# Performance work log

Hardware: AMD Instinct MI355X
Metric: run time of the kernel (lower is better)

The kernel has to match this reference:

```python
import jax, jax.numpy as jnp
import numpy as np

CH = 512      # input channels
V = 320       # codewords per group
G = 2         # groups
CV_DIM = 256  # codevector_dim (wav2vec2 default)
D = CV_DIM // G
TAU = 2.0     # gumbel temperature


def setup_inputs() -> dict:
    key = jax.random.key(0)
    k1, k2, k3, k4 = jax.random.split(key, 4)
    B, T = 32, 1024
    x = jax.random.normal(k1, (B, T, CH), jnp.float32)
    W_proj = jax.random.normal(k2, (CH, G * V), jnp.float32) / np.sqrt(CH)
    b_proj = jnp.zeros((G * V,), jnp.float32)
    codevectors = jax.random.normal(k3, (G, V, D), jnp.float32) * 0.02
    # uniform noise, transformed to Gumbel inside reference
    u_noise = jax.random.uniform(k4, (B, T, G, V), jnp.float32,
                                 minval=1e-6, maxval=1.0 - 1e-6)
    return {"x": x, "W_proj": W_proj, "b_proj": b_proj,
            "codevectors": codevectors, "u_noise": u_noise}


def reference(x, W_proj, b_proj, codevectors, u_noise):
    B, T, _ = x.shape
    # projection to per-group logits: [B,T,G,V]
    logits = (x @ W_proj + b_proj).reshape(B, T, G, V)
    # gumbel-softmax (hard, straight-through)
    g = -jnp.log(-jnp.log(u_noise))
    soft = jax.nn.softmax((logits + g) / TAU, axis=-1)
    hard = jax.nn.one_hot(jnp.argmax(soft, axis=-1), V, dtype=soft.dtype)
    st = hard + soft - jax.lax.stop_gradient(soft)
    # combine selected codewords per group, concat groups -> [B,T,CV_DIM]
    out = jnp.einsum('btgv,gvd->btgd', st, codevectors).reshape(B, T, G * D)
    return out
```

## Files before the change

kernel.cpp:

```cpp
#include <hip/hip_runtime.h>
#include <cmath>

namespace {

typedef _Float16 half8 __attribute__((ext_vector_type(8)));
typedef float f32x4 __attribute__((ext_vector_type(4)));

constexpr int M_TOTAL = 32 * 1024;
constexpr int K_CH    = 512;
constexpr int NV      = 640;
constexpr int D_CV    = 128;
constexpr int NSLOT   = 10;

constexpr int BM = 128, BN = 128, BK = 32;
constexpr int NTILE  = NV / BN;
constexpr int NPANEL = M_TOTAL / BM;
constexpr int NBLK   = NTILE * NPANEL;
constexpr int KT     = K_CH / BK;

constexpr float LO_SCALE = 4096.0f;
constexpr float LO_INV   = 1.0f / 4096.0f;

__device__ __forceinline__ void gld16(const void* g, void* l) {
  __builtin_amdgcn_global_load_lds(
      (__attribute__((address_space(1))) void*)g,
      (__attribute__((address_space(3))) void*)l, 16, 0, 0);
}

__global__ __launch_bounds__(256)
void prep_w(const float* __restrict__ W, _Float16* __restrict__ Wth,
            _Float16* __restrict__ Wtl)
{
  __shared__ float tile[32][33];
  const int bk = blockIdx.x & 15;
  const int bn = blockIdx.x >> 4;
  const int k0 = bk * 32, n0 = bn * 32;
  const int t = threadIdx.x;
  const int nn = t & 31, kk = t >> 5;
  #pragma unroll
  for (int p = 0; p < 4; ++p)
    tile[kk + p * 8][nn] = W[(size_t)(k0 + kk + p * 8) * NV + n0 + nn];
  __syncthreads();
  const int kx = t & 31, nx = t >> 5;
  #pragma unroll
  for (int p = 0; p < 4; ++p) {
    const float v = tile[kx][nx + p * 8];
    const _Float16 h = (_Float16)v;
    const _Float16 l = (_Float16)((v - (float)h) * LO_SCALE);
    const size_t o = (size_t)(n0 + nx + p * 8) * K_CH + k0 + kx;
    Wth[o] = h;
    Wtl[o] = l;
  }
}

__global__ __launch_bounds__(256, 2)
void gvq_mfma12(const float* __restrict__ x,
                const _Float16* __restrict__ Wth, const _Float16* __restrict__ Wtl,
                const float* __restrict__ bias, const float* __restrict__ u,
                float* __restrict__ pval, int* __restrict__ pidx)
{
  __shared__ __align__(16) char lds[2][32768];

  const int chunk = NBLK / 8;
  const int nid   = (blockIdx.x % 8) * chunk + blockIdx.x / 8;
  const int panel = nid / NTILE, ntile = nid % NTILE;
  const int m0 = panel * BM, n0 = ntile * BN;

  const int t    = threadIdx.x;
  const int wv   = t >> 6, lane = t & 63;
  const int wr   = wv >> 1, wc = wv & 1;
  const int li   = lane & 15, q = lane >> 4;

  const int gca = (t & 7) ^ ((t >> 3) & 7);
  const float* pxa = x + (size_t)(m0 + (t >> 3)) * K_CH + gca * 4;
  const int gcb = (t & 3) ^ ((t >> 3) & 3);
  const _Float16* pbh = Wth + (size_t)(n0 + (t >> 2)) * K_CH + gcb * 8;
  const _Float16* pbl = Wtl + (size_t)(n0 + (t >> 2)) * K_CH + gcb * 8;

  f32x4 acc1[4][4];
  f32x4 acc2[4][4];
  #pragma unroll
  for (int i = 0; i < 4; ++i)
    #pragma unroll
    for (int j = 0; j < 4; ++j) {
      acc1[i][j] = (f32x4){0.f, 0.f, 0.f, 0.f};
      acc2[i][j] = (f32x4){0.f, 0.f, 0.f, 0.f};
    }

  auto stage = [&](int kt, int b) {
    const int ko = kt * BK;
    char* L = lds[b];
    #pragma unroll
    for (int i = 0; i < 4; ++i)
      gld16(pxa + (size_t)i * 32 * K_CH + ko, L + i * 4096 + wv * 1024);
    #pragma unroll
    for (int i = 0; i < 2; ++i) {
      gld16(pbh + (size_t)i * 64 * K_CH + ko, L + 16384 + i * 4096 + wv * 1024);
      gld16(pbl + (size_t)i * 64 * K_CH + ko, L + 24576 + i * 4096 + wv * 1024);
    }
  };

  const int abase = (wr * 64 + li) * 128;
  const int s0 = (((q * 2 + 0) ^ (li & 7)) << 4);
  const int s1 = (((q * 2 + 1) ^ (li & 7)) << 4);
  const int bboff = (wc * 64 + li) * 64 + ((q ^ ((li >> 1) & 3)) << 4);

  stage(0, 0);
  stage(1, 1);
  #pragma unroll
  for (int kt = 0; kt < KT; ++kt) {
    const int cur = kt & 1;
    if (kt < KT - 1) asm volatile("s_waitcnt vmcnt(8)" ::: "memory");
    else             asm volatile("s_waitcnt vmcnt(0)" ::: "memory");
    __builtin_amdgcn_s_barrier();
    __builtin_amdgcn_sched_barrier(0);

    const char* L = lds[cur];
    half8 bh[4], bl[4];
    f32x4 af0[4], af1[4];
    #pragma unroll
    for (int fn = 0; fn < 4; ++fn) {
      bh[fn] = *reinterpret_cast<const half8*>(L + 16384 + fn * 1024 + bboff);
      bl[fn] = *reinterpret_cast<const half8*>(L + 24576 + fn * 1024 + bboff);
    }
    #pragma unroll
    for (int fm = 0; fm < 4; ++fm) {
      af0[fm] = *reinterpret_cast<const f32x4*>(L + abase + fm * 2048 + s0);
      af1[fm] = *reinterpret_cast<const f32x4*>(L + abase + fm * 2048 + s1);
    }
    #pragma unroll
    for (int fm = 0; fm < 4; ++fm) {
      half8 ah, al;
      #pragma unroll
      for (int e = 0; e < 4; ++e) {
        const float v0 = af0[fm][e], v1 = af1[fm][e];
        const _Float16 h0 = (_Float16)v0, h1 = (_Float16)v1;
        ah[e]     = h0; al[e]     = (_Float16)((v0 - (float)h0) * LO_SCALE);
        ah[4 + e] = h1; al[4 + e] = (_Float16)((v1 - (float)h1) * LO_SCALE);
      }
      #pragma unroll
      for (int fn = 0; fn < 4; ++fn) {
        acc1[fm][fn] = __builtin_amdgcn_mfma_f32_16x16x32_f16(
            ah, bh[fn], acc1[fm][fn], 0, 0, 0);
        acc2[fm][fn] = __builtin_amdgcn_mfma_f32_16x16x32_f16(
            ah, bl[fn], acc2[fm][fn], 0, 0, 0);
        acc2[fm][fn] = __builtin_amdgcn_mfma_f32_16x16x32_f16(
            al, bh[fn], acc2[fm][fn], 0, 0, 0);
      }
    }
    __builtin_amdgcn_s_barrier();
    __builtin_amdgcn_sched_barrier(0);
    if (kt + 2 < KT) stage(kt + 2, cur);
  }

  const int colbase = n0 + wc * 64 + li;
  float bb[4];
  #pragma unroll
  for (int fn = 0; fn < 4; ++fn) bb[fn] = bias[colbase + fn * 16];

  const int slot = ntile * 2 + wc;
  #pragma unroll
  for (int fm = 0; fm < 4; ++fm) {
    #pragma unroll
    for (int r = 0; r < 4; ++r) {
      const int m = m0 + wr * 64 + fm * 16 + q * 4 + r;
      float bv = -INFINITY;
      int   bi = 0x7fffffff;
      #pragma unroll
      for (int fn = 0; fn < 4; ++fn) {
        const float uu  = u[(size_t)m * NV + colbase + fn * 16];
        const float g   = -__logf(-__logf(uu));
        const float val = acc1[fm][fn][r] + acc2[fm][fn][r] * LO_INV
                          + bb[fn] + g;
        const int   n   = colbase + fn * 16;
        if (val > bv) { bv = val; bi = n; }
      }
      #pragma unroll
      for (int s = 1; s <= 8; s <<= 1) {
        const float ov = __shfl_xor(bv, s);
        const int   oi = __shfl_xor(bi, s);
        if (ov > bv || (ov == bv && oi < bi)) { bv = ov; bi = oi; }
      }
      if (li == 0) {
        pval[(size_t)m * NSLOT + slot] = bv;
        pidx[(size_t)m * NSLOT + slot] = bi;
      }
    }
  }
}

__global__ __launch_bounds__(256)
void gvq_gather(const float* __restrict__ pval,
                const int*   __restrict__ pidx,
                const float* __restrict__ cv,
                float* __restrict__ out)
{
  const int tid  = threadIdx.x;
  const int w    = tid >> 6;
  const int lane = tid & 63;
  const int m    = blockIdx.x * 4 + w;
  const int g    = lane >> 5;

  const float* pv = &pval[(size_t)m * NSLOT + g * 5];
  const int*   pi = &pidx[(size_t)m * NSLOT + g * 5];
  float bv = pv[0];
  int   bi = pi[0];
  #pragma unroll
  for (int s = 1; s < 5; ++s) {
    const float v = pv[s];
    const int   i = pi[s];
    if (v > bv || (v == bv && i < bi)) { bv = v; bi = i; }
  }
  const float4 src = *reinterpret_cast<const float4*>(
      &cv[(size_t)bi * D_CV + (lane & 31) * 4]);
  *reinterpret_cast<float4*>(&out[(size_t)m * 256 + lane * 4]) = src;
}

}

extern "C" void kernel_launch(void* const* d_in, const int* in_sizes, int n_in,
                              void* d_out, int out_size, void* d_ws, size_t ws_size,
                              hipStream_t stream)
{
  const float* x    = (const float*)d_in[0];
  const float* W    = (const float*)d_in[1];
  const float* bias = (const float*)d_in[2];
  const float* cv   = (const float*)d_in[3];
  const float* u    = (const float*)d_in[4];
  float* out = (float*)d_out;

  _Float16* Wth  = (_Float16*)d_ws;
  _Float16* Wtl  = Wth + (size_t)NV * K_CH;
  float*    pval = (float*)(Wtl + (size_t)NV * K_CH);
  int*      pidx = (int*)(pval + (size_t)M_TOTAL * NSLOT);

  hipLaunchKernelGGL(prep_w, dim3(320), dim3(256), 0, stream, W, Wth, Wtl);
  hipLaunchKernelGGL(gvq_mfma12, dim3(NBLK), dim3(256), 0, stream,
                     x, Wth, Wtl, bias, u, pval, pidx);
  hipLaunchKernelGGL(gvq_gather, dim3(M_TOTAL / 4), dim3(256), 0, stream,
                     pval, pidx, cv, out);
}
```

Measured before the change: 123.7 us.

## Replace split-fp16 GEMM with single fp16 pass plus fp32 fixup of near-ties

Drops the hi/lo fp16 split that needed three MFMAs per tile and computes logits with one fp16 MFMA, converting x to fp16 in registers before writing it to LDS. It also doubles BK. To keep the argmax correct, the kernel tracks the runner-up value per row. Rows whose top-two margin is within a tolerance are appended to a list via an atomic counter, and a fix kernel recomputes their logits in fp32. This cuts MFMA work roughly threefold and halves B traffic. The cost is two extra launches, a memset, and correctness that depends on the tolerance bounding the fp16 error.

```diff
diff --git a/kernel.cpp b/kernel.cpp
--- a/kernel.cpp
+++ b/kernel.cpp
@@ -12,14 +12,13 @@
 constexpr int D_CV    = 128;
 constexpr int NSLOT   = 10;
 
-constexpr int BM = 128, BN = 128, BK = 32;
+constexpr int BM = 128, BN = 128, BK = 64;
 constexpr int NTILE  = NV / BN;
 constexpr int NPANEL = M_TOTAL / BM;
 constexpr int NBLK   = NTILE * NPANEL;
 constexpr int KT     = K_CH / BK;
 
-constexpr float LO_SCALE = 4096.0f;
-constexpr float LO_INV   = 1.0f / 4096.0f;
+constexpr float TAU = 6e-3f;
 
 __device__ __forceinline__ void gld16(const void* g, void* l) {
   __builtin_amdgcn_global_load_lds(
@@ -28,8 +27,8 @@
 }
 
 __global__ __launch_bounds__(256)
-void prep_w(const float* __restrict__ W, _Float16* __restrict__ Wth,
-            _Float16* __restrict__ Wtl)
+void prep_w2(const float* __restrict__ W, _Float16* __restrict__ Wth,
+             float* __restrict__ Wtf)
 {
   __shared__ float tile[32][33];
   const int bk = blockIdx.x & 15;
@@ -45,19 +44,17 @@
   #pragma unroll
   for (int p = 0; p < 4; ++p) {
     const float v = tile[kx][nx + p * 8];
-    const _Float16 h = (_Float16)v;
-    const _Float16 l = (_Float16)((v - (float)h) * LO_SCALE);
     const size_t o = (size_t)(n0 + nx + p * 8) * K_CH + k0 + kx;
-    Wth[o] = h;
-    Wtl[o] = l;
+    Wth[o] = (_Float16)v;
+    Wtf[o] = v;
   }
 }
 
 __global__ __launch_bounds__(256, 2)
-void gvq_mfma12(const float* __restrict__ x,
-                const _Float16* __restrict__ Wth, const _Float16* __restrict__ Wtl,
-                const float* __restrict__ bias, const float* __restrict__ u,
-                float* __restrict__ pval, int* __restrict__ pidx)
+void gvq_p1(const float* __restrict__ x, const _Float16* __restrict__ Wth,
+            const float* __restrict__ bias, const float* __restrict__ u,
+            float* __restrict__ pval, int* __restrict__ pidx,
+            float* __restrict__ psec)
 {
   __shared__ __align__(16) char lds[2][32768];
 
@@ -71,86 +68,81 @@
   const int wr   = wv >> 1, wc = wv & 1;
   const int li   = lane & 15, q = lane >> 4;
 
-  const int gca = (t & 7) ^ ((t >> 3) & 7);
-  const float* pxa = x + (size_t)(m0 + (t >> 3)) * K_CH + gca * 4;
-  const int gcb = (t & 3) ^ ((t >> 3) & 3);
-  const _Float16* pbh = Wth + (size_t)(n0 + (t >> 2)) * K_CH + gcb * 8;
-  const _Float16* pbl = Wtl + (size_t)(n0 + (t >> 2)) * K_CH + gcb * 8;
-
-  f32x4 acc1[4][4];
-  f32x4 acc2[4][4];
+  const int ar0   = t >> 3;
+  const int aslot = (t & 7) ^ ((t >> 3) & 7);
+  const float* pxa = x + (size_t)(m0 + ar0) * K_CH + (t & 7) * 8;
+  const int bgc = (t & 7) ^ ((t >> 3) & 7);
+  const _Float16* pbh = Wth + (size_t)(n0 + (t >> 3)) * K_CH + bgc * 8;
+
+  f32x4 acc[4][4];
   #pragma unroll
   for (int i = 0; i < 4; ++i)
     #pragma unroll
-    for (int j = 0; j < 4; ++j) {
-      acc1[i][j] = (f32x4){0.f, 0.f, 0.f, 0.f};
-      acc2[i][j] = (f32x4){0.f, 0.f, 0.f, 0.f};
-    }
-
-  auto stage = [&](int kt, int b) {
-    const int ko = kt * BK;
-    char* L = lds[b];
+    for (int j = 0; j < 4; ++j) acc[i][j] = (f32x4){0.f, 0.f, 0.f, 0.f};
+
+  f32x4 aR[8];
+  auto issueA = [&](int kt) {
     #pragma unroll
     for (int i = 0; i < 4; ++i)
-      gld16(pxa + (size_t)i * 32 * K_CH + ko, L + i * 4096 + wv * 1024);
-    #pragma unroll
-    for (int i = 0; i < 2; ++i) {
-      gld16(pbh + (size_t)i * 64 * K_CH + ko, L + 16384 + i * 4096 + wv * 1024);
-      gld16(pbl + (size_t)i * 64 * K_CH + ko, L + 24576 + i * 4096 + wv * 1024);
-    }
+      #pragma unroll
+      for (int j = 0; j < 2; ++j)
+        aR[i * 2 + j] = *reinterpret_cast<const f32x4*>(
+            pxa + (size_t)i * 32 * K_CH + kt * BK + j * 4);
   };
-
-  const int abase = (wr * 64 + li) * 128;
-  const int s0 = (((q * 2 + 0) ^ (li & 7)) << 4);
-  const int s1 = (((q * 2 + 1) ^ (li & 7)) << 4);
-  const int bboff = (wc * 64 + li) * 64 + ((q ^ ((li >> 1) & 3)) << 4);
-
-  stage(0, 0);
-  stage(1, 1);
+  auto issueB = [&](int kt, int b) {
+    char* Lb = lds[b] + 16384;
+    #pragma unroll
+    for (int i = 0; i < 4; ++i)
+      gld16(pbh + (size_t)i * 32 * K_CH + kt * BK, Lb + i * 4096 + wv * 1024);
+  };
+  auto writeA = [&](int b) {
+    char* La = lds[b];
+    #pragma unroll
+    for (int i = 0; i < 4; ++i) {
+      half8 h;
+      #pragma unroll
+      for (int e = 0; e < 4; ++e) {
+        h[e]     = (_Float16)aR[i * 2][e];
+        h[4 + e] = (_Float16)aR[i * 2 + 1][e];
+      }
+      *reinterpret_cast<half8*>(La + (i * 32 + ar0) * 128 + aslot * 16) = h;
+    }
+  };
+
+  const int arow = (wr * 64 + li) * 128;
+  const int brow = 16384 + (wc * 64 + li) * 128;
+
+  issueA(0);
+  issueB(0, 0);
   #pragma unroll
   for (int kt = 0; kt < KT; ++kt) {
     const int cur = kt & 1;
-    if (kt < KT - 1) asm volatile("s_waitcnt vmcnt(8)" ::: "memory");
-    else             asm volatile("s_waitcnt vmcnt(0)" ::: "memory");
+    writeA(cur);
+    if (kt + 1 < KT) { issueA(kt + 1); issueB(kt + 1, cur ^ 1); }
+    if (kt + 1 < KT) asm volatile("s_waitcnt vmcnt(12) lgkmcnt(0)" ::: "memory");
+    else             asm volatile("s_waitcnt vmcnt(0) lgkmcnt(0)"  ::: "memory");
     __builtin_amdgcn_s_barrier();
     __builtin_amdgcn_sched_barrier(0);
 
     const char* L = lds[cur];
-    half8 bh[4], bl[4];
-    f32x4 af0[4], af1[4];
-    #pragma unroll
-    for (int fn = 0; fn < 4; ++fn) {
-      bh[fn] = *reinterpret_cast<const half8*>(L + 16384 + fn * 1024 + bboff);
-      bl[fn] = *reinterpret_cast<const half8*>(L + 24576 + fn * 1024 + bboff);
-    }
-    #pragma unroll
-    for (int fm = 0; fm < 4; ++fm) {
-      af0[fm] = *reinterpret_cast<const f32x4*>(L + abase + fm * 2048 + s0);
-      af1[fm] = *reinterpret_cast<const f32x4*>(L + abase + fm * 2048 + s1);
-    }
-    #pragma unroll
-    for (int fm = 0; fm < 4; ++fm) {
-      half8 ah, al;
-      #pragma unroll
-      for (int e = 0; e < 4; ++e) {
-        const float v0 = af0[fm][e], v1 = af1[fm][e];
-        const _Float16 h0 = (_Float16)v0, h1 = (_Float16)v1;
-        ah[e]     = h0; al[e]     = (_Float16)((v0 - (float)h0) * LO_SCALE);
-        ah[4 + e] = h1; al[4 + e] = (_Float16)((v1 - (float)h1) * LO_SCALE);
-      }
-      #pragma unroll
-      for (int fn = 0; fn < 4; ++fn) {
-        acc1[fm][fn] = __builtin_amdgcn_mfma_f32_16x16x32_f16(
-            ah, bh[fn], acc1[fm][fn], 0, 0, 0);
-        acc2[fm][fn] = __builtin_amdgcn_mfma_f32_16x16x32_f16(
-            ah, bl[fn], acc2[fm][fn], 0, 0, 0);
-        acc2[fm][fn] = __builtin_amdgcn_mfma_f32_16x16x32_f16(
-            al, bh[fn], acc2[fm][fn], 0, 0, 0);
-      }
-    }
+    #pragma unroll
+    for (int ksub = 0; ksub < 2; ++ksub) {
+      const int soff = (((ksub * 4 + q) ^ (li & 7)) << 4);
+      half8 ah[4], bh[4];
+      #pragma unroll
+      for (int f = 0; f < 4; ++f) {
+        ah[f] = *reinterpret_cast<const half8*>(L + arow + f * 2048 + soff);
+        bh[f] = *reinterpret_cast<const half8*>(L + brow + f * 2048 + soff);
+      }
+      #pragma unroll
+      for (int fm = 0; fm < 4; ++fm)
+        #pragma unroll
+        for (int fn = 0; fn < 4; ++fn)
+          acc[fm][fn] = __builtin_amdgcn_mfma_f32_16x16x32_f16(
+              ah[fm], bh[fn], acc[fm][fn], 0, 0, 0);
+    }
+    __builtin_amdgcn_sched_barrier(0);
     __builtin_amdgcn_s_barrier();
-    __builtin_amdgcn_sched_barrier(0);
-    if (kt + 2 < KT) stage(kt + 2, cur);
   }
 
   const int colbase = n0 + wc * 64 + li;
@@ -164,36 +156,41 @@
     #pragma unroll
     for (int r = 0; r < 4; ++r) {
       const int m = m0 + wr * 64 + fm * 16 + q * 4 + r;
-      float bv = -INFINITY;
-      int   bi = 0x7fffffff;
+      float v1 = -INFINITY, v2 = -INFINITY;
+      int   i1 = 0x7fffffff;
       #pragma unroll
       for (int fn = 0; fn < 4; ++fn) {
         const float uu  = u[(size_t)m * NV + colbase + fn * 16];
-        const float g   = -__logf(-__logf(uu));
-        const float val = acc1[fm][fn][r] + acc2[fm][fn][r] * LO_INV
-                          + bb[fn] + g;
+        const float gg  = -__logf(-__logf(uu));
+        const float val = acc[fm][fn][r] + bb[fn] + gg;
         const int   n   = colbase + fn * 16;
-        if (val > bv) { bv = val; bi = n; }
+        if (val > v1)      { v2 = v1; v1 = val; i1 = n; }
+        else if (val > v2) { v2 = val; }
       }
       #pragma unroll
       for (int s = 1; s <= 8; s <<= 1) {
-        const float ov = __shfl_xor(bv, s);
-        const int   oi = __shfl_xor(bi, s);
-        if (ov > bv || (ov == bv && oi < bi)) { bv = ov; bi = oi; }
+        const float ov1 = __shfl_xor(v1, s);
+        const int   oi1 = __shfl_xor(i1, s);
+        const float ov2 = __shfl_xor(v2, s);
+        const bool  win = (v1 > ov1) || (v1 == ov1 && i1 < oi1);
+        const float mv2 = fmaxf(v2, ov2);
+        if (win) { v2 = fmaxf(mv2, ov1); }
+        else     { v2 = fmaxf(mv2, v1); v1 = ov1; i1 = oi1; }
       }
       if (li == 0) {
-        pval[(size_t)m * NSLOT + slot] = bv;
-        pidx[(size_t)m * NSLOT + slot] = bi;
+        pval[(size_t)m * NSLOT + slot] = v1;
+        pidx[(size_t)m * NSLOT + slot] = i1;
+        psec[(size_t)m * NSLOT + slot] = v2;
       }
     }
   }
 }
 
 __global__ __launch_bounds__(256)
-void gvq_gather(const float* __restrict__ pval,
-                const int*   __restrict__ pidx,
-                const float* __restrict__ cv,
-                float* __restrict__ out)
+void gvq_gather3(const float* __restrict__ pval, const int* __restrict__ pidx,
+                 const float* __restrict__ psec, const float* __restrict__ cv,
+                 float* __restrict__ out, int* __restrict__ flagCnt,
+                 int* __restrict__ flagList)
 {
   const int tid  = threadIdx.x;
   const int w    = tid >> 6;
@@ -201,19 +198,79 @@
   const int m    = blockIdx.x * 4 + w;
   const int g    = lane >> 5;
 
-  const float* pv = &pval[(size_t)m * NSLOT + g * 5];
-  const int*   pi = &pidx[(size_t)m * NSLOT + g * 5];
-  float bv = pv[0];
-  int   bi = pi[0];
+  const size_t base = (size_t)m * NSLOT + g * 5;
+  float bv = pval[base], sec = -INFINITY;
+  int   bi = pidx[base], bs = 0;
   #pragma unroll
   for (int s = 1; s < 5; ++s) {
-    const float v = pv[s];
-    const int   i = pi[s];
-    if (v > bv || (v == bv && i < bi)) { bv = v; bi = i; }
+    const float v = pval[base + s];
+    const int   i = pidx[base + s];
+    if (v > bv || (v == bv && i < bi)) { sec = fmaxf(sec, bv); bv = v; bi = i; bs = s; }
+    else                               { sec = fmaxf(sec, v); }
+  }
+  sec = fmaxf(sec, psec[base + bs]);
+
+  if ((lane & 31) == 0 && (bv - sec) <= TAU) {
+    const int idx = atomicAdd(flagCnt, 1);
+    flagList[idx] = m * 2 + g;
   }
   const float4 src = *reinterpret_cast<const float4*>(
       &cv[(size_t)bi * D_CV + (lane & 31) * 4]);
   *reinterpret_cast<float4*>(&out[(size_t)m * 256 + lane * 4]) = src;
+}
+
+__global__ __launch_bounds__(256)
+void gvq_fix(const float* __restrict__ x, const float* __restrict__ Wtf,
+             const float* __restrict__ bias, const float* __restrict__ u,
+             const float* __restrict__ cv, float* __restrict__ out,
+             const int* __restrict__ flagCnt, const int* __restrict__ flagList)
+{
+  __shared__ float xs[4][K_CH];
+  const int w    = threadIdx.x >> 6;
+  const int lane = threadIdx.x & 63;
+  const int nW   = gridDim.x * 4;
+  const int wid  = blockIdx.x * 4 + w;
+  const int cnt  = *flagCnt;
+
+  for (int it = wid; it < cnt; it += nW) {
+    const int id = flagList[it];
+    const int m = id >> 1, g = id & 1;
+    {
+      f32x4* dst = reinterpret_cast<f32x4*>(xs[w]);
+      const f32x4* src = reinterpret_cast<const f32x4*>(x + (size_t)m * K_CH);
+      dst[lane]      = src[lane];
+      dst[lane + 64] = src[lane + 64];
+    }
+    float bvv = -INFINITY;
+    int   bn  = 0x7fffffff;
+    #pragma unroll 1
+    for (int c = 0; c < 5; ++c) {
+      const int n = g * 320 + c * 64 + lane;
+      const float* wt = Wtf + (size_t)n * K_CH;
+      float acc = 0.f;
+      for (int k = 0; k < K_CH; k += 4) {
+        acc = fmaf(xs[w][k + 0], wt[k + 0], acc);
+        acc = fmaf(xs[w][k + 1], wt[k + 1], acc);
+        acc = fmaf(xs[w][k + 2], wt[k + 2], acc);
+        acc = fmaf(xs[w][k + 3], wt[k + 3], acc);
+      }
+      const float uu  = u[(size_t)m * NV + n];
+      const float gg  = -logf(-logf(uu));
+      const float val = acc + bias[n] + gg;
+      if (val > bvv) { bvv = val; bn = n; }
+    }
+    #pragma unroll
+    for (int s = 1; s <= 32; s <<= 1) {
+      const float ov = __shfl_xor(bvv, s);
+      const int   oi = __shfl_xor(bn, s);
+      if (ov > bvv || (ov == bvv && oi < bn)) { bvv = ov; bn = oi; }
+    }
+    if (lane < 32) {
+      const float4 src = *reinterpret_cast<const float4*>(
+          &cv[(size_t)bn * D_CV + lane * 4]);
+      *reinterpret_cast<float4*>(&out[(size_t)m * 256 + g * 128 + lane * 4]) = src;
+    }
+  }
 }
 
 }
@@ -229,14 +286,20 @@
   const float* u    = (const float*)d_in[4];
   float* out = (float*)d_out;
 
-  _Float16* Wth  = (_Float16*)d_ws;
-  _Float16* Wtl  = Wth + (size_t)NV * K_CH;
-  float*    pval = (float*)(Wtl + (size_t)NV * K_CH);
-  int*      pidx = (int*)(pval + (size_t)M_TOTAL * NSLOT);
-
-  hipLaunchKernelGGL(prep_w, dim3(320), dim3(256), 0, stream, W, Wth, Wtl);
-  hipLaunchKernelGGL(gvq_mfma12, dim3(NBLK), dim3(256), 0, stream,
-                     x, Wth, Wtl, bias, u, pval, pidx);
-  hipLaunchKernelGGL(gvq_gather, dim3(M_TOTAL / 4), dim3(256), 0, stream,
-                     pval, pidx, cv, out);
-}
+  _Float16* Wth   = (_Float16*)d_ws;
+  float*    Wtf   = (float*)(Wth + (size_t)NV * K_CH);
+  float*    pval  = Wtf + (size_t)NV * K_CH;
+  int*      pidx  = (int*)(pval + (size_t)M_TOTAL * NSLOT);
+  float*    psec  = (float*)(pidx + (size_t)M_TOTAL * NSLOT);
+  int*      flagCnt  = (int*)(psec + (size_t)M_TOTAL * NSLOT);
+  int*      flagList = flagCnt + 4;
+
+  hipMemsetAsync(flagCnt, 0, sizeof(int), stream);
+  hipLaunchKernelGGL(prep_w2, dim3(320), dim3(256), 0, stream, W, Wth, Wtf);
+  hipLaunchKernelGGL(gvq_p1, dim3(NBLK), dim3(256), 0, stream,
+                     x, Wth, bias, u, pval, pidx, psec);
+  hipLaunchKernelGGL(gvq_gather3, dim3(M_TOTAL / 4), dim3(256), 0, stream,
+                     pval, pidx, psec, cv, out, flagCnt, flagList);
+  hipLaunchKernelGGL(gvq_fix, dim3(128), dim3(256), 0, stream,
+                     x, Wtf, bias, u, cv, out, flagCnt, flagList);
+}
```

New measurement: 202.1 us. 63.3% more time.
